# Performance work log

Hardware: AMD Instinct MI355X
Metric: run time of the kernel (lower is better)

Reference implementation:

```python
import jax, jax.numpy as jnp
import numpy as np

FRACTION_BITS = 16
INTEGER_BITS = 16


def round_to_fixed(x):
    # floor-quantize to 2^-16 steps, clamp to signed 16-bit integer range
    delta = 2.0 ** (-FRACTION_BITS)
    bound = 2.0 ** (INTEGER_BITS - 1)
    return jnp.clip(jnp.floor(x / delta) * delta, -bound, bound - 1.0)


def setup_inputs() -> dict:
    key = jax.random.key(0)
    k1, k2, k3, k4 = jax.random.split(key, 4)
    N, IN_F, OUT_F = 4096, 4096, 4096
    inp = jax.random.normal(k1, (N, IN_F), dtype=jnp.float32)
    # reset_parameters: shift ~ U(-10,-1), sign ~ U(-1,0), bias ~ U(-b,b), b=1/sqrt(fan_in)
    shift = jax.random.uniform(k2, (OUT_F, IN_F), minval=-10.0, maxval=-1.0, dtype=jnp.float32)
    sign = jax.random.uniform(k3, (OUT_F, IN_F), minval=-1.0, maxval=0.0, dtype=jnp.float32)
    b = 1.0 / np.sqrt(IN_F)
    bias = jax.random.uniform(k4, (OUT_F,), minval=-b, maxval=b, dtype=jnp.float32)
    return {"input": inp, "shift": shift, "sign": sign, "bias": bias}


def reference(input, shift, sign, bias):
    # eager (non-kernel) path of LinearShiftFunction.forward
    q_in = round_to_fixed(input)
    q_bias = round_to_fixed(bias)
    s = jnp.clip(sign, -1.0, 1.0)
    v = jnp.exp2(jnp.round(shift)) * jnp.sign(s)  # [out_f, in_f] power-of-two weights
    out = q_in @ v.T + q_bias[None, :]
    return out
```

## Files before the change

kernel.cpp:

```cpp
#include <hip/hip_runtime.h>
#include <hip/hip_bf16.h>


#define BM 256
#define BN 256
#define BK 64

typedef __bf16 bf16_t;
typedef __attribute__((ext_vector_type(8))) __bf16 bf16x8;
typedef __attribute__((ext_vector_type(4))) __bf16 bf16x4;
typedef __attribute__((ext_vector_type(4))) float f32x4;

__device__ __forceinline__ float q16(float x) {
    float f = floorf(x * 65536.0f) * (1.0f / 65536.0f);
    return fminf(fmaxf(f, -32768.0f), 32767.0f);
}

__global__ void quant_input_kernel(const float* __restrict__ in,
                                   bf16_t* __restrict__ out, int nvec) {
    int stride = gridDim.x * blockDim.x;
    for (int i = blockIdx.x * blockDim.x + threadIdx.x; i < nvec; i += stride) {
        float4 v = reinterpret_cast<const float4*>(in)[i];
        bf16x4 o;
        o[0] = (bf16_t)q16(v.x);
        o[1] = (bf16_t)q16(v.y);
        o[2] = (bf16_t)q16(v.z);
        o[3] = (bf16_t)q16(v.w);
        reinterpret_cast<bf16x4*>(out)[i] = o;
    }
}

__global__ void make_weight_kernel(const float* __restrict__ shift,
                                   const float* __restrict__ sign_,
                                   bf16_t* __restrict__ out, int nvec) {
    int stride = gridDim.x * blockDim.x;
    for (int i = blockIdx.x * blockDim.x + threadIdx.x; i < nvec; i += stride) {
        float4 sh = reinterpret_cast<const float4*>(shift)[i];
        float4 sg = reinterpret_cast<const float4*>(sign_)[i];
        float shs[4] = {sh.x, sh.y, sh.z, sh.w};
        float sgs[4] = {sg.x, sg.y, sg.z, sg.w};
        bf16x4 o;
#pragma unroll
        for (int j = 0; j < 4; ++j) {
            float s = fminf(fmaxf(sgs[j], -1.0f), 1.0f);
            float sv = (s > 0.0f) ? 1.0f : ((s < 0.0f) ? -1.0f : 0.0f);
            o[j] = (bf16_t)(exp2f(rintf(shs[j])) * sv);
        }
        reinterpret_cast<bf16x4*>(out)[i] = o;
    }
}


#define STAGE(LDSOFF, SRC) do {                                                          \
    const bf16_t* _s = (SRC);                                                            \
    bf16_t* _d = &lds[(LDSOFF)] + tid * 8;                                               \
    __builtin_amdgcn_global_load_lds((const __attribute__((address_space(1))) void*)_s,  \
                                     (__attribute__((address_space(3))) void*)_d,        \
                                     16, 0, 0);                                          \
    __builtin_amdgcn_global_load_lds(                                                    \
        (const __attribute__((address_space(1))) void*)(_s + (size_t)64 * K),            \
        (__attribute__((address_space(3))) void*)(_d + 4096), 16, 0, 0);                 \
} while (0)

#define READ_A(BUF, MH) do {                                                             \
    const bf16_t* _As = &lds[(BUF) * 32768 + wm * 8192];                                 \
    _Pragma("unroll") for (int m = 0; m < 4; ++m)                                        \
        _Pragma("unroll") for (int kk = 0; kk < 2; ++kk)                                 \
            af[m][kk] = *(const bf16x8*)&_As[((MH) * 64 + m * 16 + fr) * 64 +            \
                                             ((((kk << 2) | hi) ^ fr7) << 3)];           \
} while (0)

#define READ_B(BUF, NH, BF) do {                                                         \
    const bf16_t* _Bs = &lds[(BUF) * 32768 + 16384 + (wn >> 1) * 8192];                  \
    _Pragma("unroll") for (int n = 0; n < 2; ++n)                                        \
        _Pragma("unroll") for (int kk = 0; kk < 2; ++kk)                                 \
            BF[n][kk] = *(const bf16x8*)&_Bs[((wn & 1) * 64 + ((NH) * 2 + n) * 16 + fr)  \
                                                 * 64 +                                  \
                                             ((((kk << 2) | hi) ^ fr7) << 3)];           \
} while (0)

#define QUAD(MH, NH, BF) do {                                                            \
    _Pragma("unroll") for (int m = 0; m < 4; ++m)                                        \
        _Pragma("unroll") for (int n = 0; n < 2; ++n)                                    \
            _Pragma("unroll") for (int kk = 0; kk < 2; ++kk)                             \
                acc[(MH) * 4 + m][(NH) * 2 + n] =                                        \
                    __builtin_amdgcn_mfma_f32_16x16x32_bf16(                             \
                        af[m][kk], BF[n][kk], acc[(MH) * 4 + m][(NH) * 2 + n], 0, 0, 0); \
} while (0)

#define PH_SYNC_MFMA(MH, NH, BF)                                                         \
    __builtin_amdgcn_s_barrier();                                                        \
    asm volatile("s_waitcnt lgkmcnt(0)" ::: "memory");                                   \
    __builtin_amdgcn_sched_barrier(0);                                                   \
    __builtin_amdgcn_s_setprio(1);                                                       \
    QUAD(MH, NH, BF);                                                                    \
    __builtin_amdgcn_s_setprio(0);

#define TILE(BUF, T, S01, S23, ENDW) do {                                                \
                                                                 \
    READ_A(BUF, 0);                                                                      \
    READ_B(BUF, 0, b0f);                                                                 \
    if (S01) STAGE(((BUF) ^ 1) * 32768 + 3 * 8192, srcB1 + (size_t)((T) + 1) * 64);      \
    PH_SYNC_MFMA(0, 0, b0f)                                                              \
    __builtin_amdgcn_s_barrier(); __builtin_amdgcn_sched_barrier(0);                     \
                                                                 \
    READ_B(BUF, 1, b1f);                                                                 \
    if (S01) STAGE(((BUF) ^ 1) * 32768 + 1 * 8192, srcA1 + (size_t)((T) + 1) * 64);      \
    PH_SYNC_MFMA(0, 1, b1f)                                                              \
    __builtin_amdgcn_s_barrier(); __builtin_amdgcn_sched_barrier(0);                     \
                                                                 \
    READ_A(BUF, 1);                                                                      \
    if (S23) STAGE((BUF) * 32768 + 2 * 8192, srcB0 + (size_t)((T) + 2) * 64);            \
    PH_SYNC_MFMA(1, 0, b0f)                                                              \
    __builtin_amdgcn_s_barrier(); __builtin_amdgcn_sched_barrier(0);                     \
                                   \
    if (S23) STAGE((BUF) * 32768 + 0 * 8192, srcA0 + (size_t)((T) + 2) * 64);            \
    PH_SYNC_MFMA(1, 1, b1f)                                                              \
    if ((ENDW) == 4) asm volatile("s_waitcnt vmcnt(4)" ::: "memory");                    \
    if ((ENDW) == 0) asm volatile("s_waitcnt vmcnt(0)" ::: "memory");                    \
    __builtin_amdgcn_s_barrier(); __builtin_amdgcn_sched_barrier(0);                     \
} while (0)

__global__ __launch_bounds__(512, 2)
void gemm256_kernel(const bf16_t* __restrict__ A,
                    const bf16_t* __restrict__ B,
                    const float* __restrict__ bias,
                    float* __restrict__ C,
                    int M, int N, int K) {
    __shared__ bf16_t lds[65536];

    const int ntn = N / BN;
    const int nwg = gridDim.x;
    const int q = nwg >> 3, r = nwg & 7;
    const int xcd = blockIdx.x & 7, lid = blockIdx.x >> 3;
    const int swz = (xcd < r ? xcd * (q + 1) : r * (q + 1) + (xcd - r) * q) + lid;
    const int tile_m = (swz / ntn) * BM;
    const int tile_n = (swz % ntn) * BN;

    const int tid = threadIdx.x;
    const int lane = tid & 63;
    const int wid = tid >> 6;
    const int wm = wid >> 2;
    const int wn = wid & 3;
    const int fr = lane & 15;
    const int hi = lane >> 4;
    const int fr7 = fr & 7;

    const int colsrc_e = ((((tid & 7) * 16) ^ ((tid & 56) << 1)) >> 1);
    const bf16_t* srcA0 = A + (size_t)(tile_m + (tid >> 3)) * K + colsrc_e;
    const bf16_t* srcA1 = srcA0 + (size_t)128 * K;
    const bf16_t* srcB0 = B + (size_t)(tile_n + (tid >> 3)) * K + colsrc_e;
    const bf16_t* srcB1 = srcB0 + (size_t)128 * K;

    bf16x8 af[4][2], b0f[2][2], b1f[2][2];
    f32x4 acc[8][4] = {};

    STAGE(16384, srcB0);
    STAGE(0, srcA0);
    STAGE(24576, srcB1);
    STAGE(8192, srcA1);
    STAGE(32768 + 16384, srcB0 + 64);
    STAGE(32768 + 0, srcA0 + 64);
    asm volatile("s_waitcnt vmcnt(4)" ::: "memory");
    __builtin_amdgcn_s_barrier();
    __builtin_amdgcn_sched_barrier(0);

    const int npairs = K / 128;
    for (int i = 0; i < npairs - 1; ++i) {
        TILE(0, 2 * i, 1, 1, 4);
        TILE(1, 2 * i + 1, 1, 1, 4);
    }
    TILE(0, 2 * npairs - 2, 1, 0, 0);
    TILE(1, 2 * npairs - 1, 0, 0, -1);

    float qb[4];
#pragma unroll
    for (int ng = 0; ng < 4; ++ng)
        qb[ng] = q16(bias[tile_n + wn * 64 + ng * 16 + fr]);
#pragma unroll
    for (int mg = 0; mg < 8; ++mg) {
        const int grow0 = tile_m + wm * 128 + mg * 16 + hi * 4;
#pragma unroll
        for (int ng = 0; ng < 4; ++ng) {
            const int gcol = tile_n + wn * 64 + ng * 16 + fr;
#pragma unroll
            for (int rr = 0; rr < 4; ++rr)
                C[(size_t)(grow0 + rr) * N + gcol] = acc[mg][ng][rr] + qb[ng];
        }
    }
}

extern "C" void kernel_launch(void* const* d_in, const int* in_sizes, int n_in,
                              void* d_out, int out_size, void* d_ws, size_t ws_size,
                              hipStream_t stream) {
    const float* inp   = (const float*)d_in[0];
    const float* shift = (const float*)d_in[1];
    const float* sign_ = (const float*)d_in[2];
    const float* bias  = (const float*)d_in[3];
    float* out = (float*)d_out;

    const int OUT_F = in_sizes[3];
    const int IN_F  = in_sizes[1] / OUT_F;
    const int Mrows = in_sizes[0] / IN_F;

    bf16_t* Aq = (bf16_t*)d_ws;
    bf16_t* Wq = Aq + (size_t)Mrows * IN_F;

    const int nA = Mrows * IN_F;
    const int nW = OUT_F * IN_F;

    quant_input_kernel<<<2048, 256, 0, stream>>>(inp, Aq, nA >> 2);
    make_weight_kernel<<<2048, 256, 0, stream>>>(shift, sign_, Wq, nW >> 2);

    dim3 grid((Mrows / BM) * (OUT_F / BN));
    gemm256_kernel<<<grid, 512, 0, stream>>>(Aq, Wq, bias, out,
                                             Mrows, OUT_F, IN_F);
}
```

Baseline: 162.3 us.

## Restage full tile two ahead into same buffer and drop explicit LDS waits

Reworks the software pipeline of the 256x256 bf16 GEMM main loop. Previously the upper A/B quarters of the next tile went into the other buffer and the lower quarters of tile T+2 into the current one. Now all four quarters of tile T+2 are issued into the current buffer during the last two phases, with the vmcnt threshold raised to match. The explicit lgkmcnt(0) waits and sched_barriers around each MFMA phase are replaced by plain barriers with compiler memory fences. This lets the compiler place LDS-read waits itself and interleave more freely. The trade-off is a shorter window for some loads to land, and scheduling that now depends on what the compiler chooses.

```diff
diff --git a/kernel.cpp b/kernel.cpp
--- a/kernel.cpp
+++ b/kernel.cpp
@@ -51,6 +51,9 @@
 }
 
 
+#define VMW(N) asm volatile("s_waitcnt vmcnt(" #N ")" ::: "memory")
+#define BARF() do { __builtin_amdgcn_s_barrier(); asm volatile("" ::: "memory"); } while (0)
+
 #define STAGE(LDSOFF, SRC) do {                                                          \
     const bf16_t* _s = (SRC);                                                            \
     bf16_t* _d = &lds[(LDSOFF)] + tid * 8;                                               \
@@ -88,37 +91,42 @@
                         af[m][kk], BF[n][kk], acc[(MH) * 4 + m][(NH) * 2 + n], 0, 0, 0); \
 } while (0)
 
-#define PH_SYNC_MFMA(MH, NH, BF)                                                         \
-    __builtin_amdgcn_s_barrier();                                                        \
-    asm volatile("s_waitcnt lgkmcnt(0)" ::: "memory");                                   \
-    __builtin_amdgcn_sched_barrier(0);                                                   \
+#define MFMA_PH(MH, NH, BF)                                                              \
     __builtin_amdgcn_s_setprio(1);                                                       \
     QUAD(MH, NH, BF);                                                                    \
     __builtin_amdgcn_s_setprio(0);
 
-#define TILE(BUF, T, S01, S23, ENDW) do {                                                \
-                                                                 \
+#define TILE(BUF, T, S, ENDW) do {                                                      \
+                                                                            \
     READ_A(BUF, 0);                                                                      \
     READ_B(BUF, 0, b0f);                                                                 \
-    if (S01) STAGE(((BUF) ^ 1) * 32768 + 3 * 8192, srcB1 + (size_t)((T) + 1) * 64);      \
-    PH_SYNC_MFMA(0, 0, b0f)                                                              \
-    __builtin_amdgcn_s_barrier(); __builtin_amdgcn_sched_barrier(0);                     \
-                                                                 \
+    BARF();                                                                              \
+    MFMA_PH(0, 0, b0f)                                                                   \
+    BARF();                                                                              \
+                                                                            \
     READ_B(BUF, 1, b1f);                                                                 \
-    if (S01) STAGE(((BUF) ^ 1) * 32768 + 1 * 8192, srcA1 + (size_t)((T) + 1) * 64);      \
-    PH_SYNC_MFMA(0, 1, b1f)                                                              \
-    __builtin_amdgcn_s_barrier(); __builtin_amdgcn_sched_barrier(0);                     \
-                                                                 \
+    BARF();                                                                              \
+    MFMA_PH(0, 1, b1f)                                                                   \
+    BARF();                                                                              \
+                        \
     READ_A(BUF, 1);                                                                      \
-    if (S23) STAGE((BUF) * 32768 + 2 * 8192, srcB0 + (size_t)((T) + 2) * 64);            \
-    PH_SYNC_MFMA(1, 0, b0f)                                                              \
-    __builtin_amdgcn_s_barrier(); __builtin_amdgcn_sched_barrier(0);                     \
-                                   \
-    if (S23) STAGE((BUF) * 32768 + 0 * 8192, srcA0 + (size_t)((T) + 2) * 64);            \
-    PH_SYNC_MFMA(1, 1, b1f)                                                              \
-    if ((ENDW) == 4) asm volatile("s_waitcnt vmcnt(4)" ::: "memory");                    \
-    if ((ENDW) == 0) asm volatile("s_waitcnt vmcnt(0)" ::: "memory");                    \
-    __builtin_amdgcn_s_barrier(); __builtin_amdgcn_sched_barrier(0);                     \
+    if (S) {                                                                             \
+        STAGE((BUF) * 32768 + 2 * 8192, srcB0 + (size_t)((T) + 2) * 64);                 \
+        STAGE((BUF) * 32768 + 3 * 8192, srcB1 + (size_t)((T) + 2) * 64);                 \
+    }                                                                                    \
+    BARF();                                                                              \
+    MFMA_PH(1, 0, b0f)                                                                   \
+    BARF();                                                                              \
+                                    \
+    if (S) {                                                                             \
+        STAGE((BUF) * 32768 + 0 * 8192, srcA0 + (size_t)((T) + 2) * 64);                 \
+        STAGE((BUF) * 32768 + 1 * 8192, srcA1 + (size_t)((T) + 2) * 64);                 \
+    }                                                                                    \
+    BARF();                                                                              \
+    MFMA_PH(1, 1, b1f)                                                                   \
+    if ((ENDW) == 8) VMW(8);                                                             \
+    else if ((ENDW) == 0) VMW(0);                                                        \
+    BARF();                                                                              \
 } while (0)
 
 __global__ __launch_bounds__(512, 2)
@@ -156,22 +164,23 @@
     f32x4 acc[8][4] = {};
 
     STAGE(16384, srcB0);
+    STAGE(24576, srcB1);
     STAGE(0, srcA0);
-    STAGE(24576, srcB1);
     STAGE(8192, srcA1);
     STAGE(32768 + 16384, srcB0 + 64);
+    STAGE(32768 + 24576, srcB1 + 64);
     STAGE(32768 + 0, srcA0 + 64);
-    asm volatile("s_waitcnt vmcnt(4)" ::: "memory");
-    __builtin_amdgcn_s_barrier();
-    __builtin_amdgcn_sched_barrier(0);
+    STAGE(32768 + 8192, srcA1 + 64);
+    VMW(8);
+    BARF();
 
     const int npairs = K / 128;
     for (int i = 0; i < npairs - 1; ++i) {
-        TILE(0, 2 * i, 1, 1, 4);
-        TILE(1, 2 * i + 1, 1, 1, 4);
-    }
-    TILE(0, 2 * npairs - 2, 1, 0, 0);
-    TILE(1, 2 * npairs - 1, 0, 0, -1);
+        TILE(0, 2 * i, 1, 8);
+        TILE(1, 2 * i + 1, 1, 8);
+    }
+    TILE(0, 2 * npairs - 2, 0, 0);
+    TILE(1, 2 * npairs - 1, 0, -1);
 
     float qb[4];
 #pragma unroll
```

Result: slower. 166.1 us (+2.4%).
